# Kernel tuning notes

Hardware: AMD Instinct MI355X
Metric: run time of the kernel (lower is better)

## Reference

```python
import jax, jax.numpy as jnp
import numpy as np

B, A, F, H = 64, 128, 32, 64


def setup_inputs() -> dict:
    key = jax.random.key(0)
    ks = jax.random.split(key, 16)
    def dense(k, fan_in, fan_out):
        return jax.random.normal(k, (fan_in, fan_out), jnp.float32) / np.sqrt(fan_in)
    inp = {
        "X": jax.random.normal(ks[0], (B, A, F), jnp.float32),
        "mask": jax.random.randint(ks[1], (B, A), 0, 2, jnp.int32),
        # base MLP: F -> H -> H -> 1
        "base_W1": dense(ks[2], F, H), "base_b1": jnp.zeros((H,), jnp.float32),
        "base_W2": dense(ks[3], H, H), "base_b2": jnp.zeros((H,), jnp.float32),
        "base_W3": dense(ks[4], H, 1), "base_b3": jnp.zeros((1,), jnp.float32),
        # pair MLP: 2F -> H -> H -> 1
        "pair_W1": dense(ks[5], 2 * F, H), "pair_b1": jnp.zeros((H,), jnp.float32),
        "pair_W2": dense(ks[6], H, H), "pair_b2": jnp.zeros((H,), jnp.float32),
        "pair_W3": dense(ks[7], H, 1), "pair_b3": jnp.zeros((1,), jnp.float32),
    }
    return inp


def reference(X, mask, base_W1, base_b1, base_W2, base_b2, base_W3, base_b3,
              pair_W1, pair_b1, pair_W2, pair_b2, pair_W3, pair_b3):
    f = X.shape[-1]
    a = X.shape[1]
    # base utility f_base(x_i): (B,A)
    hb = jax.nn.relu(jnp.einsum('baf,fh->bah', X, base_W1) + base_b1)
    hb = jax.nn.relu(jnp.einsum('bah,hk->bak', hb, base_W2) + base_b2)
    base_u = (jnp.einsum('bah,ho->bao', hb, base_W3) + base_b3)[..., 0]
    # pairwise MLP on concat([x_i, x_j]); first layer decomposed to avoid
    # materializing the (B,A,A,2F) concat: W1 = [Wi; Wj]
    Wi, Wj = pair_W1[:f], pair_W1[f:]
    hi = jnp.einsum('baf,fh->bah', X, Wi)  # contribution of x_i
    hj = jnp.einsum('baf,fh->bah', X, Wj)  # contribution of x_j
    h = jax.nn.relu(hi[:, :, None, :] + hj[:, None, :, :] + pair_b1)  # (B,A,A,H)
    h = jax.nn.relu(jnp.einsum('bijh,hk->bijk', h, pair_W2) + pair_b2)
    pe = (jnp.einsum('bijh,ho->bijo', h, pair_W3) + pair_b3)[..., 0]  # (B,A,A)
    # zero out diagonal (j != i)
    pe = pe * (1.0 - jnp.eye(a, dtype=pe.dtype))
    # availability mask on both i and j
    mf = mask.astype(pe.dtype)
    pe = pe * (mf[:, :, None] * mf[:, None, :])
    utilities = base_u + jnp.sum(pe, axis=-1)
    utilities = jnp.where(mask.astype(bool), utilities, jnp.float32(-1e9))
    return jax.nn.softmax(utilities, axis=-1)
```

## Files before the change

### kernel.cpp

```cpp
#include <hip/hip_runtime.h>
#include <hip/hip_bf16.h>

#define BB 64
#define AA 128
#define FF 32
#define HH 64

typedef float  f32x4  __attribute__((ext_vector_type(4)));
typedef float  f32x16 __attribute__((ext_vector_type(16)));
typedef __bf16 bf16x8 __attribute__((ext_vector_type(8)));
typedef unsigned int uint4v __attribute__((ext_vector_type(4)));

#define OFF_HIP   0
#define OFF_HJ    524288
#define OFF_BU    1048576
#define OFF_UTIL  1056768
#define OFF_W2FH  1064960
#define OFF_W2FL  1067008
#define OFF_JLIST 1069056
#define OFF_JCNT  1077248

static __device__ __forceinline__ unsigned short f2b_rne(float x) {
    __hip_bfloat16 h = __float2bfloat16(x);
    return __builtin_bit_cast(unsigned short, h);
}
static __device__ __forceinline__ float b2f(unsigned short u) {
    unsigned v = ((unsigned)u) << 16;
    return __builtin_bit_cast(float, v);
}

__global__ __launch_bounds__(64)
void ddc_features(const float* __restrict__ X, const int* __restrict__ mask,
                  const float* __restrict__ bW1, const float* __restrict__ bb1,
                  const float* __restrict__ bW2, const float* __restrict__ bb2,
                  const float* __restrict__ bW3, const float* __restrict__ bb3,
                  const float* __restrict__ pW1, const float* __restrict__ pb1,
                  const float* __restrict__ pW2,
                  float* __restrict__ hi_p, float* __restrict__ hj,
                  float* __restrict__ base_u,
                  unsigned short* __restrict__ W2fh,
                  unsigned short* __restrict__ W2fl,
                  int* __restrict__ jlist, int* __restrict__ jcnt) {
    const int a = blockIdx.x, b = blockIdx.y, lane = threadIdx.x;
    const int row = b * AA + a;

    const float* __restrict__ x = X + row * FF;
    float xr[FF];
#pragma unroll
    for (int f = 0; f < FF; ++f) xr[f] = x[f];

    float vhi = pb1[lane];
    float vhj = 0.f;
    float v1  = bb1[lane];
#pragma unroll
    for (int f = 0; f < FF; ++f) {
        vhi = fmaf(xr[f], pW1[f * HH + lane], vhi);
        vhj = fmaf(xr[f], pW1[(FF + f) * HH + lane], vhj);
        v1  = fmaf(xr[f], bW1[f * HH + lane], v1);
    }
    v1 = fmaxf(v1, 0.f);

    float v2 = bb2[lane];
#pragma unroll
    for (int k = 0; k < HH; ++k) {
        float hk = __shfl(v1, k);
        v2 = fmaf(hk, bW2[k * HH + lane], v2);
    }
    v2 = fmaxf(v2, 0.f);

    float bu = v2 * bW3[lane];
#pragma unroll
    for (int off = 32; off; off >>= 1) bu += __shfl_xor(bu, off);

    hi_p[row * HH + lane] = vhi;
    hj  [row * HH + lane] = vhj;
    if (lane == 0) base_u[row] = bu + bb3[0];

    if (a == 0) {
        int base0 = 0;
#pragma unroll
        for (int hlf = 0; hlf < 2; ++hlf) {
            int idx = hlf * 64 + lane;
            int m = mask[b * AA + idx];
            unsigned long long bal = __ballot(m != 0);
            int pos = __popcll(bal & ((1ull << lane) - 1ull));
            if (m) jlist[b * AA + base0 + pos] = idx;
            base0 += (int)__popcll(bal);
        }
        if (lane == 0) jcnt[b] = base0;
    }

    if (a == 1 && b == 0) {
        const int col = lane & 31, half = lane >> 5;
#pragma unroll
        for (int fid = 0; fid < 8; ++fid) {
            const int nt = fid >> 2, ks = fid & 3;
            const int n = nt * 32 + col;
            const int ko = ks * 16 + half * 8;
#pragma unroll
            for (int e = 0; e < 8; ++e) {
                float w = pW2[(ko + e) * HH + n];
                unsigned short uh = f2b_rne(w);
                W2fh[(fid * 64 + lane) * 8 + e] = uh;
                W2fl[(fid * 64 + lane) * 8 + e] = f2b_rne(w - b2f(uh));
            }
        }
    }
}

#define SPLIT_PAIR(pa, pb, outh, outl)                                   \
    {   unsigned ua = __builtin_bit_cast(unsigned, pa);                  \
        unsigned ub = __builtin_bit_cast(unsigned, pb);                  \
        outh = (ua >> 16) | (ub & 0xFFFF0000u);                          \
        float ra = pa - __builtin_bit_cast(float, ua & 0xFFFF0000u);     \
        float rb = pb - __builtin_bit_cast(float, ub & 0xFFFF0000u);     \
        unsigned va = __builtin_bit_cast(unsigned, ra);                  \
        unsigned vb = __builtin_bit_cast(unsigned, rb);                  \
        outl = (va >> 16) | (vb & 0xFFFF0000u); }

__global__ __launch_bounds__(256, 2)
void ddc_pairs_mfma(const float* __restrict__ hi_p, const float* __restrict__ hj,
                    const float* __restrict__ base_u,
                    const int* __restrict__ jlist, const int* __restrict__ jcnt,
                    const unsigned short* __restrict__ W2fh,
                    const unsigned short* __restrict__ W2fl,
                    const float* __restrict__ pb2, const float* __restrict__ pW3,
                    const float* __restrict__ pb3, float* __restrict__ util) {
    __shared__ float sHJ[AA][HH + 4];

    const int t  = threadIdx.x;
    const int gx = blockIdx.x;
    const int b  = blockIdx.y;
    const int cnt = jcnt[b];
    const int ngroups = (cnt + 3) >> 2;
    if (gx >= ngroups) return;

    const int l = t & 63, wid = t >> 6;
    const int col = l & 31, half = l >> 5;

#define LOADB(nt, ks, vh, vl)                                               \
    uint4v vh = *(const uint4v*)(W2fh + (((nt) * 4 + (ks)) * 64 + l) * 8);  \
    uint4v vl = *(const uint4v*)(W2fl + (((nt) * 4 + (ks)) * 64 + l) * 8);
    LOADB(0, 0, bh00, bl00)
    LOADB(0, 1, bh01, bl01)
    LOADB(0, 2, bh02, bl02)
    LOADB(0, 3, bh03, bl03)
    LOADB(1, 0, bh10, bl10)
    LOADB(1, 1, bh11, bl11)
    LOADB(1, 2, bh12, bl12)
    LOADB(1, 3, bh13, bl13)
#undef LOADB

    {
        const int r = t >> 1, hf = t & 1;
        f32x4* dst = (f32x4*)&sHJ[r][hf * 32];
        if (r < cnt) {
            const int jr = jlist[b * AA + r];
            const f32x4* __restrict__ src =
                (const f32x4*)(hj + (b * AA + jr) * HH + hf * 32);
#pragma unroll
            for (int q = 0; q < 8; ++q) dst[q] = src[q];
        } else {
#pragma unroll
            for (int q = 0; q < 8; ++q) dst[q] = (f32x4)0.f;
        }
    }

    __syncthreads();

#define PIN(v) asm("" : "+a"(v));
    PIN(bh00) PIN(bl00) PIN(bh01) PIN(bl01)
    PIN(bh02) PIN(bl02) PIN(bh03) PIN(bl03)
    PIN(bh10) PIN(bl10) PIN(bh11) PIN(bl11)
    PIN(bh12) PIN(bl12) PIN(bh13) PIN(bl13)
#undef PIN

    const float b2v0 = pb2[col], b2v1 = pb2[32 + col];
    const float w3v0 = pW3[col], w3v1 = pW3[32 + col];
    const float b3s  = pb3[0] * (1.f / 32.f);

    const int ntiles = (cnt + 31) >> 5;

    for (int g = gx; g < ngroups; g += 8) {
        const int slot = g * 4 + wid;
        if (slot >= cnt) continue;
        const int i = __builtin_amdgcn_readfirstlane(jlist[b * AA + slot]);

        const float* __restrict__ hp = hi_p + (b * AA + i) * HH;
        f32x4 yv[8];
#pragma unroll
        for (int ks = 0; ks < 4; ++ks) {
            const int ko = ks * 16 + half * 8;
            yv[2 * ks]     = *(const f32x4*)(hp + ko);
            yv[2 * ks + 1] = *(const f32x4*)(hp + ko + 4);
        }

        float tsum = 0.f;
        for (int jt = 0; jt < ntiles; ++jt) {
            f32x16 acc0 = b2v0, acc1 = b2v1;
            const int jj = jt * 32 + col;

#define KSTEP(ks, BH0, BL0, BH1, BL1)                                       \
            {   const int ko = (ks) * 16 + half * 8;                        \
                f32x4 x0 = *(const f32x4*)&sHJ[jj][ko];                     \
                f32x4 x1 = *(const f32x4*)&sHJ[jj][ko + 4];                 \
                f32x4 y0 = yv[2 * (ks)], y1 = yv[2 * (ks) + 1];             \
                float h0 = fmaxf(x0[0] + y0[0], 0.f);                       \
                float h1 = fmaxf(x0[1] + y0[1], 0.f);                       \
                float h2 = fmaxf(x0[2] + y0[2], 0.f);                       \
                float h3 = fmaxf(x0[3] + y0[3], 0.f);                       \
                float h4 = fmaxf(x1[0] + y1[0], 0.f);                       \
                float h5 = fmaxf(x1[1] + y1[1], 0.f);                       \
                float h6 = fmaxf(x1[2] + y1[2], 0.f);                       \
                float h7 = fmaxf(x1[3] + y1[3], 0.f);                       \
                unsigned a01, a23, a45, a67, c01, c23, c45, c67;            \
                SPLIT_PAIR(h0, h1, a01, c01)                                \
                SPLIT_PAIR(h2, h3, a23, c23)                                \
                SPLIT_PAIR(h4, h5, a45, c45)                                \
                SPLIT_PAIR(h6, h7, a67, c67)                                \
                uint4v ahv = {a01, a23, a45, a67};                          \
                uint4v alv = {c01, c23, c45, c67};                          \
                bf16x8 ah = __builtin_bit_cast(bf16x8, ahv);                \
                bf16x8 al = __builtin_bit_cast(bf16x8, alv);                \
                acc0 = __builtin_amdgcn_mfma_f32_32x32x16_bf16(             \
                    al, __builtin_bit_cast(bf16x8, BH0), acc0, 0, 0, 0);    \
                acc1 = __builtin_amdgcn_mfma_f32_32x32x16_bf16(             \
                    al, __builtin_bit_cast(bf16x8, BH1), acc1, 0, 0, 0);    \
                acc0 = __builtin_amdgcn_mfma_f32_32x32x16_bf16(             \
                    ah, __builtin_bit_cast(bf16x8, BL0), acc0, 0, 0, 0);    \
                acc1 = __builtin_amdgcn_mfma_f32_32x32x16_bf16(             \
                    ah, __builtin_bit_cast(bf16x8, BL1), acc1, 0, 0, 0);    \
                acc0 = __builtin_amdgcn_mfma_f32_32x32x16_bf16(             \
                    ah, __builtin_bit_cast(bf16x8, BH0), acc0, 0, 0, 0);    \
                acc1 = __builtin_amdgcn_mfma_f32_32x32x16_bf16(             \
                    ah, __builtin_bit_cast(bf16x8, BH1), acc1, 0, 0, 0);    \
            }
            KSTEP(0, bh00, bl00, bh10, bl10)
            KSTEP(1, bh01, bl01, bh11, bl11)
            KSTEP(2, bh02, bl02, bh12, bl12)
            KSTEP(3, bh03, bl03, bh13, bl13)
#undef KSTEP

#pragma unroll
            for (int r = 0; r < 16; ++r) {
                const int rrow = (r & 3) + 8 * (r >> 2) + 4 * half;
                const int jg = jt * 32 + rrow;
                float v = fmaxf(acc0[r], 0.f) * w3v0 +
                          fmaxf(acc1[r], 0.f) * w3v1 + b3s;
                const bool valid = (jg < cnt) && (jg != slot);
                tsum += valid ? v : 0.f;
            }
        }
#pragma unroll
        for (int off = 32; off; off >>= 1) tsum += __shfl_xor(tsum, off);
        if (l == 0) util[b * AA + i] = base_u[b * AA + i] + tsum;
    }
}

__global__ __launch_bounds__(64)
void ddc_softmax(const float* __restrict__ util, const int* __restrict__ mask,
                 float* __restrict__ out) {
    const int b = blockIdx.x, lane = threadIdx.x;
    const int r0 = b * AA + lane, r1 = r0 + 64;
    const float u0 = (mask[r0] != 0) ? util[r0] : -1e9f;
    const float u1 = (mask[r1] != 0) ? util[r1] : -1e9f;

    float m = fmaxf(u0, u1);
#pragma unroll
    for (int off = 32; off; off >>= 1) m = fmaxf(m, __shfl_xor(m, off));

    const float e0 = __expf(u0 - m);
    const float e1 = __expf(u1 - m);
    float s = e0 + e1;
#pragma unroll
    for (int off = 32; off; off >>= 1) s += __shfl_xor(s, off);

    const float inv = 1.f / s;
    out[r0] = e0 * inv;
    out[r1] = e1 * inv;
}

extern "C" void kernel_launch(void* const* d_in, const int* in_sizes, int n_in,
                              void* d_out, int out_size, void* d_ws, size_t ws_size,
                              hipStream_t stream) {
    const float* X    = (const float*)d_in[0];
    const int*   mask = (const int*)  d_in[1];
    const float* bW1  = (const float*)d_in[2];
    const float* bb1  = (const float*)d_in[3];
    const float* bW2  = (const float*)d_in[4];
    const float* bb2  = (const float*)d_in[5];
    const float* bW3  = (const float*)d_in[6];
    const float* bb3  = (const float*)d_in[7];
    const float* pW1  = (const float*)d_in[8];
    const float* pb1  = (const float*)d_in[9];
    const float* pW2  = (const float*)d_in[10];
    const float* pb2  = (const float*)d_in[11];
    const float* pW3  = (const float*)d_in[12];
    const float* pb3  = (const float*)d_in[13];

    float* ws    = (float*)d_ws;
    float* hi_p  = ws + OFF_HIP;
    float* hjW   = ws + OFF_HJ;
    float* baseu = ws + OFF_BU;
    float* util  = ws + OFF_UTIL;
    unsigned short* W2fh = (unsigned short*)(ws + OFF_W2FH);
    unsigned short* W2fl = (unsigned short*)(ws + OFF_W2FL);
    int*   jlist = (int*)(ws + OFF_JLIST);
    int*   jcnt  = (int*)(ws + OFF_JCNT);

    float* out = (float*)d_out;

    dim3 g1(AA, BB);
    ddc_features<<<g1, 64, 0, stream>>>(X, mask, bW1, bb1, bW2, bb2, bW3, bb3,
                                        pW1, pb1, pW2,
                                        hi_p, hjW, baseu, W2fh, W2fl,
                                        jlist, jcnt);
    dim3 g2(8, BB);
    ddc_pairs_mfma<<<g2, 256, 0, stream>>>(hi_p, hjW, baseu, jlist, jcnt,
                                           W2fh, W2fl, pb2, pW3, pb3, util);
    ddc_softmax<<<BB, 64, 0, stream>>>(util, mask, out);
}
```

Measured before the change: 40.22 us.

## Stage W2 fragments in LDS to cut registers and raise pair-kernel occupancy

The pair MLP kernel no longer keeps the 16 bf16 hi/lo W2 fragments pinned in AGPRs. They are copied once per block into shared memory and reloaded from LDS inside each k-step, with an opaque zero offset that stops the compiler from hoisting the loads back out. This frees registers so launch bounds can allow 3 blocks per CU, and the grid widens from 8 to 12 blocks per batch to spread the work. The cost is extra LDS traffic in the inner MFMA loop and a larger shared-memory footprint per block. There is also more per-block setup, since each block now copies the weights into LDS.

```diff
diff --git a/kernel.cpp b/kernel.cpp
--- a/kernel.cpp
+++ b/kernel.cpp
@@ -5,6 +5,7 @@
 #define AA 128
 #define FF 32
 #define HH 64
+#define GXDIM 12
 
 typedef float  f32x4  __attribute__((ext_vector_type(4)));
 typedef float  f32x16 __attribute__((ext_vector_type(16)));
@@ -118,7 +119,7 @@
         unsigned vb = __builtin_bit_cast(unsigned, rb);                  \
         outl = (va >> 16) | (vb & 0xFFFF0000u); }
 
-__global__ __launch_bounds__(256, 2)
+__global__ __launch_bounds__(256, 3)
 void ddc_pairs_mfma(const float* __restrict__ hi_p, const float* __restrict__ hj,
                     const float* __restrict__ base_u,
                     const int* __restrict__ jlist, const int* __restrict__ jcnt,
@@ -126,7 +127,9 @@
                     const unsigned short* __restrict__ W2fl,
                     const float* __restrict__ pb2, const float* __restrict__ pW3,
                     const float* __restrict__ pb3, float* __restrict__ util) {
-    __shared__ float sHJ[AA][HH + 4];
+    __shared__ float  sHJ[AA][HH + 4];
+    __shared__ uint4v sBH[512];
+    __shared__ uint4v sBL[512];
 
     const int t  = threadIdx.x;
     const int gx = blockIdx.x;
@@ -138,18 +141,14 @@
     const int l = t & 63, wid = t >> 6;
     const int col = l & 31, half = l >> 5;
 
-#define LOADB(nt, ks, vh, vl)                                               \
-    uint4v vh = *(const uint4v*)(W2fh + (((nt) * 4 + (ks)) * 64 + l) * 8);  \
-    uint4v vl = *(const uint4v*)(W2fl + (((nt) * 4 + (ks)) * 64 + l) * 8);
-    LOADB(0, 0, bh00, bl00)
-    LOADB(0, 1, bh01, bl01)
-    LOADB(0, 2, bh02, bl02)
-    LOADB(0, 3, bh03, bl03)
-    LOADB(1, 0, bh10, bl10)
-    LOADB(1, 1, bh11, bl11)
-    LOADB(1, 2, bh12, bl12)
-    LOADB(1, 3, bh13, bl13)
-#undef LOADB
+    {
+        const uint4v* __restrict__ gbh = (const uint4v*)W2fh;
+        const uint4v* __restrict__ gbl = (const uint4v*)W2fl;
+        sBH[t]       = gbh[t];
+        sBH[t + 256] = gbh[t + 256];
+        sBL[t]       = gbl[t];
+        sBL[t + 256] = gbl[t + 256];
+    }
 
     {
         const int r = t >> 1, hf = t & 1;
@@ -168,20 +167,13 @@
 
     __syncthreads();
 
-#define PIN(v) asm("" : "+a"(v));
-    PIN(bh00) PIN(bl00) PIN(bh01) PIN(bl01)
-    PIN(bh02) PIN(bl02) PIN(bh03) PIN(bl03)
-    PIN(bh10) PIN(bl10) PIN(bh11) PIN(bl11)
-    PIN(bh12) PIN(bl12) PIN(bh13) PIN(bl13)
-#undef PIN
-
     const float b2v0 = pb2[col], b2v1 = pb2[32 + col];
     const float w3v0 = pW3[col], w3v1 = pW3[32 + col];
     const float b3s  = pb3[0] * (1.f / 32.f);
 
     const int ntiles = (cnt + 31) >> 5;
 
-    for (int g = gx; g < ngroups; g += 8) {
+    for (int g = gx; g < ngroups; g += GXDIM) {
         const int slot = g * 4 + wid;
         if (slot >= cnt) continue;
         const int i = __builtin_amdgcn_readfirstlane(jlist[b * AA + slot]);
@@ -197,11 +189,18 @@
 
         float tsum = 0.f;
         for (int jt = 0; jt < ntiles; ++jt) {
+            unsigned zofs = 0;
+            asm volatile("" : "+v"(zofs));
+
             f32x16 acc0 = b2v0, acc1 = b2v1;
             const int jj = jt * 32 + col;
 
-#define KSTEP(ks, BH0, BL0, BH1, BL1)                                       \
+#define KSTEP(ks)                                                           \
             {   const int ko = (ks) * 16 + half * 8;                        \
+                uint4v bh0 = sBH[(ks) * 64 + l + zofs];                     \
+                uint4v bl0 = sBL[(ks) * 64 + l + zofs];                     \
+                uint4v bh1 = sBH[(4 + (ks)) * 64 + l + zofs];               \
+                uint4v bl1 = sBL[(4 + (ks)) * 64 + l + zofs];               \
                 f32x4 x0 = *(const f32x4*)&sHJ[jj][ko];                     \
                 f32x4 x1 = *(const f32x4*)&sHJ[jj][ko + 4];                 \
                 f32x4 y0 = yv[2 * (ks)], y1 = yv[2 * (ks) + 1];             \
@@ -223,22 +222,22 @@
                 bf16x8 ah = __builtin_bit_cast(bf16x8, ahv);                \
                 bf16x8 al = __builtin_bit_cast(bf16x8, alv);                \
                 acc0 = __builtin_amdgcn_mfma_f32_32x32x16_bf16(             \
-                    al, __builtin_bit_cast(bf16x8, BH0), acc0, 0, 0, 0);    \
+                    al, __builtin_bit_cast(bf16x8, bh0), acc0, 0, 0, 0);    \
                 acc1 = __builtin_amdgcn_mfma_f32_32x32x16_bf16(             \
-                    al, __builtin_bit_cast(bf16x8, BH1), acc1, 0, 0, 0);    \
+                    al, __builtin_bit_cast(bf16x8, bh1), acc1, 0, 0, 0);    \
                 acc0 = __builtin_amdgcn_mfma_f32_32x32x16_bf16(             \
-                    ah, __builtin_bit_cast(bf16x8, BL0), acc0, 0, 0, 0);    \
+                    ah, __builtin_bit_cast(bf16x8, bl0), acc0, 0, 0, 0);    \
                 acc1 = __builtin_amdgcn_mfma_f32_32x32x16_bf16(             \
-                    ah, __builtin_bit_cast(bf16x8, BL1), acc1, 0, 0, 0);    \
+                    ah, __builtin_bit_cast(bf16x8, bl1), acc1, 0, 0, 0);    \
                 acc0 = __builtin_amdgcn_mfma_f32_32x32x16_bf16(             \
-                    ah, __builtin_bit_cast(bf16x8, BH0), acc0, 0, 0, 0);    \
+                    ah, __builtin_bit_cast(bf16x8, bh0), acc0, 0, 0, 0);    \
                 acc1 = __builtin_amdgcn_mfma_f32_32x32x16_bf16(             \
-                    ah, __builtin_bit_cast(bf16x8, BH1), acc1, 0, 0, 0);    \
+                    ah, __builtin_bit_cast(bf16x8, bh1), acc1, 0, 0, 0);    \
             }
-            KSTEP(0, bh00, bl00, bh10, bl10)
-            KSTEP(1, bh01, bl01, bh11, bl11)
-            KSTEP(2, bh02, bl02, bh12, bl12)
-            KSTEP(3, bh03, bl03, bh13, bl13)
+            KSTEP(0)
+            KSTEP(1)
+            KSTEP(2)
+            KSTEP(3)
 #undef KSTEP
 
 #pragma unroll
@@ -315,7 +314,7 @@
                                         pW1, pb1, pW2,
                                         hi_p, hjW, baseu, W2fh, W2fl,
                                         jlist, jcnt);
-    dim3 g2(8, BB);
+    dim3 g2(GXDIM, BB);
     ddc_pairs_mfma<<<g2, 256, 0, stream>>>(hi_p, hjW, baseu, jlist, jcnt,
                                            W2fh, W2fl, pb2, pW3, pb3, util);
     ddc_softmax<<<BB, 64, 0, stream>>>(util, mask, out);
```

Measured after the change: 37.97 us. 5.6% less time.
